# Optimization experiments

Measured on AMD Instinct MI355X. Metric: run time of the kernel, lower is better.

Reference implementation:

```python
import jax, jax.numpy as jnp
import numpy as np

DFAUD = 1024
DFRGB = 1024
DIM_K = 1024
N_HEADS = 4
B, T = 16, 1024


def setup_inputs() -> dict:
    key = jax.random.key(0)
    ks = jax.random.split(key, 11)
    s = lambda d: 1.0 / np.sqrt(d)
    return {
        "x": jax.random.normal(ks[0], (B, T, DFAUD), jnp.float32),
        "y": jax.random.normal(ks[1], (B, T, DFRGB), jnp.float32),
        "adj": jax.random.normal(ks[2], (B, T, T), jnp.float32),
        "Wq": jax.random.uniform(ks[3], (DIM_K, DFAUD), jnp.float32, -s(DFAUD), s(DFAUD)),
        "bq": jnp.zeros((DIM_K,), jnp.float32),
        "Wk": jax.random.uniform(ks[4], (DIM_K, DFRGB), jnp.float32, -s(DFRGB), s(DFRGB)),
        "bk": jnp.zeros((DIM_K,), jnp.float32),
        "Wv": jax.random.uniform(ks[5], (DIM_K, DFRGB), jnp.float32, -s(DFRGB), s(DFRGB)),
        "bv": jnp.zeros((DIM_K,), jnp.float32),
        "Wo": jax.random.uniform(ks[6], (DFRGB, DIM_K), jnp.float32, -s(DIM_K), s(DIM_K)),
        "bo": jnp.zeros((DFRGB,), jnp.float32),
    }


def reference(x, y, adj, Wq, bq, Wk, bk, Wv, bv, Wo, bo):
    b, t = x.shape[0], x.shape[1]
    dh = DIM_K // N_HEADS
    norm = 1.0 / np.sqrt(DIM_K)
    # Faithful reproduction of the torch reshape(-1, B, T, dim_k // n_heads):
    # [B, T, dim_k] -> [n_heads, B, T, dh] (row-major reshape, layout-mixing for h>1)
    Q = (x @ Wq.T + bq).reshape(N_HEADS, b, t, dh)
    K = (y @ Wk.T + bk).reshape(N_HEADS, b, t, dh)
    V = (y @ Wv.T + bv).reshape(N_HEADS, b, t, dh)
    scores = jnp.einsum('hbqd,hbkd->hbqk', Q, K) * norm  # [h, B, T, T]
    att = jax.nn.softmax(scores + adj, axis=-1)          # adj [B,T,T] broadcasts
    temp = jnp.einsum('hbqk,hbkd->hbqd', att, V).reshape(b, t, DIM_K)
    out = (temp @ Wo.T + bo).reshape(-1, t, y.shape[2])
    return out
```

## Files before the change

### kernel.cpp

```cpp
#include <hip/hip_runtime.h>
#include <stdint.h>

typedef unsigned short u16;
typedef __attribute__((ext_vector_type(8))) short short8_t;
typedef __attribute__((ext_vector_type(4))) float f32x4;

typedef const __attribute__((address_space(1))) void GV;
typedef __attribute__((address_space(3))) void LV;

__device__ __forceinline__ void gload_lds16(const void* g, void* l) {
  __builtin_amdgcn_global_load_lds((GV*)g, (LV*)l, 16, 0, 0);
}

__device__ __forceinline__ u16 f2bf(float f) {
  union { float f; uint32_t u; } v; v.f = f;
  return (u16)((v.u + 0x7FFFu + ((v.u >> 16) & 1u)) >> 16);
}

__device__ __forceinline__ f32x4 fz4() { f32x4 v = {0.f, 0.f, 0.f, 0.f}; return v; }

__global__ __launch_bounds__(256) void cast_kernel(const float* __restrict__ in,
                                                   u16* __restrict__ out) {
  int i = (blockIdx.x * 256 + threadIdx.x) * 4;
  float4 v = *(const float4*)(in + i);
  ushort4 o;
  o.x = f2bf(v.x); o.y = f2bf(v.y); o.z = f2bf(v.z); o.w = f2bf(v.w);
  *(ushort4*)(out + i) = o;
}

template <int OUT_BF16>
__global__ __launch_bounds__(512, 2) void gemm8(const u16* __restrict__ A,
                                                const u16* __restrict__ B,
                                                const float* __restrict__ bias,
                                                void* __restrict__ Cout,
                                                int M, int N, int K) {
  __shared__ u16 Al[2 * 16384];
  __shared__ u16 Bl[2 * 16384];
  const int tid = threadIdx.x, w = tid >> 6, l = tid & 63;
  const int g = l >> 4, q = l & 15;
  const int n0 = blockIdx.x * 256, m0 = blockIdx.y * 256;
  const int wr = (w >> 2) * 128, wc = (w & 3) * 64;
  const int NT = K >> 6;
  const int ah = w >> 2;
  const int bh = (w & 3) >> 1;
  const int brow0 = ((w & 3) & 1) * 64;

#define STAGE_A(S, half)                                                          \
  {                                                                               \
    _Pragma("unroll") for (int j_ = 0; j_ < 2; ++j_) {                            \
      const int idx_ = j_ * 512 + tid;                                            \
      const int row_ = idx_ >> 3;                                                 \
      const int sl_ = (idx_ & 7) ^ (((idx_ >> 5) & 1) << 1);                      \
      gload_lds16(A + (size_t)(m0 + (half) * 128 + row_) * K + (S) * 64 + sl_ * 8,\
                  Al + ((S) & 1) * 16384 + (half) * 8192 + (j_ * 512 + w * 64) * 8);\
    }                                                                             \
  }
#define STAGE_B(S, half)                                                          \
  {                                                                               \
    _Pragma("unroll") for (int j_ = 0; j_ < 2; ++j_) {                            \
      const int idx_ = j_ * 512 + tid;                                            \
      const int row_ = idx_ >> 3;                                                 \
      const int sl_ = (idx_ & 7) ^ (((idx_ >> 5) & 1) << 1);                      \
      gload_lds16(B + (size_t)(n0 + (half) * 128 + row_) * K + (S) * 64 + sl_ * 8,\
                  Bl + ((S) & 1) * 16384 + (half) * 8192 + (j_ * 512 + w * 64) * 8);\
    }                                                                             \
  }

  f32x4 acc[8][4];
#pragma unroll
  for (int i = 0; i < 8; ++i)
#pragma unroll
    for (int n = 0; n < 4; ++n) acc[i][n] = fz4();

  float bv[4];
#pragma unroll
  for (int nf = 0; nf < 4; ++nf) bv[nf] = bias[n0 + wc + nf * 16 + q];

  STAGE_A(0, 0); STAGE_A(0, 1); STAGE_B(0, 0); STAGE_B(0, 1);
  STAGE_A(1, 0); STAGE_A(1, 1); STAGE_B(1, 0); STAGE_B(1, 1);
  asm volatile("s_waitcnt vmcnt(8)");
  __builtin_amdgcn_s_barrier();

  short8_t bfr[4][2];
  for (int S = 0; S < NT; ++S) {
    const int bs = (S & 1) * 16384;
#pragma unroll
    for (int p = 0; p < 4; ++p) {
      short8_t afr[2][2];
#pragma unroll
      for (int mi = 0; mi < 2; ++mi)
#pragma unroll
        for (int kk = 0; kk < 2; ++kk) {
          const int r = (2 * p + mi) * 16 + q;
          afr[mi][kk] = *(const short8_t*)(Al + bs + ah * 8192 + r * 64 +
                                           ((kk * 4 + g) ^ (((r >> 2) & 1) << 1)) * 8);
        }
      if (p == 0) {
#pragma unroll
        for (int nf = 0; nf < 4; ++nf)
#pragma unroll
          for (int kk = 0; kk < 2; ++kk) {
            const int r = brow0 + nf * 16 + q;
            bfr[nf][kk] = *(const short8_t*)(Bl + bs + bh * 8192 + r * 64 +
                                             ((kk * 4 + g) ^ (((r >> 2) & 1) << 1)) * 8);
          }
      }
      if (p == 0 && S >= 1 && S + 1 < NT) STAGE_A(S + 1, 0);
      if (p == 1 && S >= 1 && S + 1 < NT) STAGE_A(S + 1, 1);
      if (p == 2 && S + 2 < NT) STAGE_B(S + 2, 0);
      if (p == 3 && S + 2 < NT) STAGE_B(S + 2, 1);
      if (p == 3) {
        if (S == NT - 2) { asm volatile("s_waitcnt vmcnt(0)"); }
        else if (S < NT - 2) { asm volatile("s_waitcnt vmcnt(4)"); }
      }
      __builtin_amdgcn_s_barrier();
      asm volatile("s_waitcnt lgkmcnt(0)" ::: "memory");
      __builtin_amdgcn_sched_barrier(0);
      __builtin_amdgcn_s_setprio(1);
#pragma unroll
      for (int nf = 0; nf < 4; ++nf)
#pragma unroll
        for (int mi = 0; mi < 2; ++mi)
#pragma unroll
          for (int kk = 0; kk < 2; ++kk)
            acc[2 * p + mi][nf] = __builtin_amdgcn_mfma_f32_16x16x32_bf16(
                afr[mi][kk], bfr[nf][kk], acc[2 * p + mi][nf], 0, 0, 0);
      __builtin_amdgcn_s_setprio(0);
      __builtin_amdgcn_s_barrier();
    }
  }
#undef STAGE_A
#undef STAGE_B

#pragma unroll
  for (int nf = 0; nf < 4; ++nf) {
    const int col = n0 + wc + nf * 16 + q;
#pragma unroll
    for (int mf = 0; mf < 8; ++mf) {
      const int rowb = m0 + wr + mf * 16 + g * 4;
#pragma unroll
      for (int j = 0; j < 4; ++j) {
        const float vv = acc[mf][nf][j] + bv[nf];
        if (OUT_BF16)
          ((u16*)Cout)[(size_t)(rowb + j) * N + col] = f2bf(vv);
        else
          ((float*)Cout)[(size_t)(rowb + j) * N + col] = vv;
      }
    }
  }
}

__global__ __launch_bounds__(256) void transpose_v(const u16* __restrict__ V,
                                                   u16* __restrict__ VT) {
  __shared__ u16 t[64][68];
  const int hb = blockIdx.z;
  const int t0 = blockIdx.x * 64, d0 = blockIdx.y * 64;
  const u16* src = V + (size_t)hb * 1024 * 256;
  u16* dst = VT + (size_t)hb * 256 * 1024;
  const int tid = threadIdx.x;
#pragma unroll
  for (int i = 0; i < 4; ++i) {
    const int idx = i * 256 + tid;
    const int r = idx >> 4, c4 = (idx & 15) * 4;
    ushort4 v = *(const ushort4*)(src + (size_t)(t0 + r) * 256 + d0 + c4);
    *(ushort4*)&t[r][c4] = v;
  }
  __syncthreads();
#pragma unroll
  for (int i = 0; i < 4; ++i) {
    const int idx = i * 256 + tid;
    const int r = idx >> 4, c4 = (idx & 15) * 4;
    ushort4 v;
    v.x = t[c4][r]; v.y = t[c4 + 1][r]; v.z = t[c4 + 2][r]; v.w = t[c4 + 3][r];
    *(ushort4*)(dst + (size_t)(d0 + r) * 1024 + t0 + c4) = v;
  }
}

__global__ __launch_bounds__(256) void attn_kernel(const u16* __restrict__ Q,
                                                   const u16* __restrict__ Kf,
                                                   const u16* __restrict__ VT,
                                                   const float* __restrict__ adj,
                                                   u16* __restrict__ O) {
  __shared__ u16 Ks[32 * 256];
  __shared__ u16 Vs[256 * 32];
  __shared__ u16 Ps[4][16 * 32];
  const int tid = threadIdx.x, w = tid >> 6, l = tid & 63;
  const int g = l >> 4, q = l & 15;
  const int bid = blockIdx.x;
  const int xcd = bid & 7, idx = bid >> 3;
  const int b = xcd * 2 + (idx >> 6);
  const int qb = (idx >> 2) & 15, h = idx & 3;
  const int hb = h * 16 + b;
  const int q0 = qb * 64;
  const u16* qb_p = Q + ((size_t)hb * 1024 + q0 + w * 16) * 256;
  const u16* kb = Kf + (size_t)hb * 1024 * 256;
  const u16* vtb = VT + (size_t)hb * 256 * 1024;
  const float* adjr = adj + (size_t)b * 1024 * 1024 + (size_t)(q0 + w * 16 + q) * 1024;

  const int krow_b = tid >> 5;
  const int kslot = tid & 31;
  const int vdr_b = tid >> 2;
  const int vsl = tid & 3;

  short8_t qf[8];
#pragma unroll
  for (int kk = 0; kk < 8; ++kk)
    qf[kk] = *(const short8_t*)(qb_p + (size_t)q * 256 + kk * 32 + g * 8);

  f32x4 o[16];
#pragma unroll
  for (int n = 0; n < 16; ++n) o[n] = fz4();
  float mrun = -1e30f, lrun = 0.f;

  short8_t kst[4], vst[4];

#define LOADREGS(ktt)                                                              \
  {                                                                                \
    _Pragma("unroll") for (int i_ = 0; i_ < 4; ++i_) {                             \
      const int row_ = i_ * 8 + krow_b;                                            \
      kst[i_] = *(const short8_t*)(kb + (size_t)((ktt) * 32 + row_) * 256 +        \
                                   kslot * 8);                                     \
    }                                                                              \
    _Pragma("unroll") for (int i_ = 0; i_ < 4; ++i_) {                             \
      const int dr_ = i_ * 64 + vdr_b;                                             \
      vst[i_] = *(const short8_t*)(vtb + (size_t)dr_ * 1024 + (ktt) * 32 +         \
                                   vsl * 8);                                       \
    }                                                                              \
  }
#define WRITEREGS()                                                                \
  {                                                                                \
    _Pragma("unroll") for (int i_ = 0; i_ < 4; ++i_) {                             \
      const int row_ = i_ * 8 + krow_b;                                            \
      *(short8_t*)((char*)Ks + row_ * 512 + ((kslot ^ (row_ & 7)) * 16)) = kst[i_];\
    }                                                                              \
    _Pragma("unroll") for (int i_ = 0; i_ < 4; ++i_) {                             \
      const int dr_ = i_ * 64 + vdr_b;                                             \
      *(short8_t*)((char*)Vs + dr_ * 64 + ((vsl ^ ((dr_ >> 1) & 3)) * 16)) = vst[i_];\
    }                                                                              \
  }

  LOADREGS(0);
  float4 a0 = *(const float4*)(adjr + 0 * 32 + 0 * 16 + g * 4);
  float4 a1 = *(const float4*)(adjr + 0 * 32 + 1 * 16 + g * 4);
  WRITEREGS();
  __syncthreads();

  for (int kt = 0; kt < 32; ++kt) {
    float4 n0v = a0, n1v = a1;
    if (kt < 31) {
      LOADREGS(kt + 1);
      n0v = *(const float4*)(adjr + (kt + 1) * 32 + 0 * 16 + g * 4);
      n1v = *(const float4*)(adjr + (kt + 1) * 32 + 1 * 16 + g * 4);
    }

    f32x4 s[2];
    __builtin_amdgcn_s_setprio(1);
#pragma unroll
    for (int f = 0; f < 2; ++f) {
      f32x4 a = fz4();
      const int row = f * 16 + q;
      const char* kr = (const char*)Ks + row * 512;
#pragma unroll
      for (int kk = 0; kk < 8; ++kk) {
        const int cb = kk * 64 + g * 16;
        short8_t kfr = *(const short8_t*)(kr + (cb ^ ((row & 7) << 4)));
        a = __builtin_amdgcn_mfma_f32_16x16x32_bf16(kfr, qf[kk], a, 0, 0, 0);
      }
      s[f] = a;
    }
    __builtin_amdgcn_s_setprio(0);

#pragma unroll
    for (int j = 0; j < 4; ++j) {
      s[0][j] = s[0][j] * 0.03125f + ((const float*)&a0)[j];
      s[1][j] = s[1][j] * 0.03125f + ((const float*)&a1)[j];
    }

    float pmax = s[0][0];
#pragma unroll
    for (int j = 1; j < 4; ++j) pmax = fmaxf(pmax, s[0][j]);
#pragma unroll
    for (int j = 0; j < 4; ++j) pmax = fmaxf(pmax, s[1][j]);
    pmax = fmaxf(pmax, __shfl_xor(pmax, 16));
    pmax = fmaxf(pmax, __shfl_xor(pmax, 32));

    if (!__all(pmax - mrun <= 8.0f)) {
      const float mn = fmaxf(mrun, pmax);
      const float al = __expf(mrun - mn);
      mrun = mn;
      lrun *= al;
#pragma unroll
      for (int n = 0; n < 16; ++n)
#pragma unroll
        for (int r = 0; r < 4; ++r) o[n][r] *= al;
    }

    float sum = 0.f;
#pragma unroll
    for (int f = 0; f < 2; ++f)
#pragma unroll
      for (int j = 0; j < 4; ++j) {
        const float p = __expf(s[f][j] - mrun);
        s[f][j] = p;
        sum += p;
      }
    sum += __shfl_xor(sum, 16);
    sum += __shfl_xor(sum, 32);
    lrun += sum;

    {
      char* pw = (char*)Ps[w] + q * 64;
      const int swz = (q >> 1) & 3;
#pragma unroll
      for (int f = 0; f < 2; ++f) {
        ushort4 pk;
        pk.x = f2bf(s[f][0]); pk.y = f2bf(s[f][1]);
        pk.z = f2bf(s[f][2]); pk.w = f2bf(s[f][3]);
        *(ushort4*)(pw + ((f * 32 + g * 8) ^ (swz << 4))) = pk;
      }
    }
    asm volatile("s_waitcnt lgkmcnt(0)");
    __builtin_amdgcn_sched_barrier(0);
    short8_t pa = *(const short8_t*)((const char*)Ps[w] + q * 64 +
                                     ((g * 16) ^ (((q >> 1) & 3) << 4)));

    __builtin_amdgcn_s_setprio(1);
#pragma unroll
    for (int n = 0; n < 16; ++n) {
      const int dr = n * 16 + q;
      const int sl = g ^ ((dr >> 1) & 3);
      short8_t vf = *(const short8_t*)((const char*)Vs + dr * 64 + sl * 16);
      o[n] = __builtin_amdgcn_mfma_f32_16x16x32_bf16(vf, pa, o[n], 0, 0, 0);
    }
    __builtin_amdgcn_s_setprio(0);

    if (kt < 31) {
      __syncthreads();
      WRITEREGS();
      __syncthreads();
    }
    a0 = n0v; a1 = n1v;
  }
#undef LOADREGS
#undef WRITEREGS

  const float inv = 1.0f / lrun;
  u16* ob = O + ((size_t)hb * 1024 + q0 + w * 16 + q) * 256;
#pragma unroll
  for (int n = 0; n < 16; ++n) {
    ushort4 st;
    st.x = f2bf(o[n][0] * inv); st.y = f2bf(o[n][1] * inv);
    st.z = f2bf(o[n][2] * inv); st.w = f2bf(o[n][3] * inv);
    *(ushort4*)(ob + n * 16 + g * 4) = st;
  }
}

extern "C" void kernel_launch(void* const* d_in, const int* in_sizes, int n_in,
                              void* d_out, int out_size, void* d_ws, size_t ws_size,
                              hipStream_t stream) {
  (void)in_sizes; (void)n_in; (void)out_size; (void)ws_size;
  const float* x   = (const float*)d_in[0];
  const float* y   = (const float*)d_in[1];
  const float* adj = (const float*)d_in[2];
  const float* Wq  = (const float*)d_in[3];
  const float* bq  = (const float*)d_in[4];
  const float* Wk  = (const float*)d_in[5];
  const float* bk  = (const float*)d_in[6];
  const float* Wv  = (const float*)d_in[7];
  const float* bv  = (const float*)d_in[8];
  const float* Wo  = (const float*)d_in[9];
  const float* bo  = (const float*)d_in[10];

  char* ws = (char*)d_ws;
  const size_t MB = 1ull << 20;
  u16* Xb  = (u16*)(ws + 0);
  u16* Yb  = (u16*)(ws + 32 * MB);
  u16* Wqb = (u16*)(ws + 64 * MB);
  u16* Wkb = (u16*)(ws + 66 * MB);
  u16* Wvb = (u16*)(ws + 68 * MB);
  u16* Wob = (u16*)(ws + 70 * MB);
  u16* Qb  = (u16*)(ws + 72 * MB);
  u16* Kb  = (u16*)(ws + 104 * MB);
  u16* Vb  = (u16*)(ws + 136 * MB);
  u16* VTb = (u16*)(ws + 168 * MB);
  u16* Tmp = Xb;

  cast_kernel<<<16384, 256, 0, stream>>>(x, Xb);
  cast_kernel<<<16384, 256, 0, stream>>>(y, Yb);
  cast_kernel<<<1024, 256, 0, stream>>>(Wq, Wqb);
  cast_kernel<<<1024, 256, 0, stream>>>(Wk, Wkb);
  cast_kernel<<<1024, 256, 0, stream>>>(Wv, Wvb);
  cast_kernel<<<1024, 256, 0, stream>>>(Wo, Wob);

  dim3 gg(4, 64);
  gemm8<1><<<gg, 512, 0, stream>>>(Xb, Wqb, bq, Qb, 16384, 1024, 1024);
  gemm8<1><<<gg, 512, 0, stream>>>(Yb, Wkb, bk, Kb, 16384, 1024, 1024);
  gemm8<1><<<gg, 512, 0, stream>>>(Yb, Wvb, bv, Vb, 16384, 1024, 1024);

  transpose_v<<<dim3(16, 4, 64), 256, 0, stream>>>(Vb, VTb);

  attn_kernel<<<1024, 256, 0, stream>>>(Qb, Kb, VTb, adj, Tmp);

  gemm8<0><<<gg, 512, 0, stream>>>(Tmp, Wob, bo, d_out, 16384, 1024, 1024);
}
```

Measured before the change: 376.0 us.

## Double the attention key tile to 64 and halve loop iterations

The flash-attention loop now processes 64 keys per iteration instead of 32. K, V and P tiles in LDS double in size, and the V/P swizzle layouts are redone for 128-byte rows. The PV product now issues two MFMAs per output fragment. This halves the number of barrier pairs and softmax-rescale passes per row block. The adj prefetch across iterations is replaced by loads at the top of each iteration, and the larger register staging and LDS footprint may reduce occupancy.

```diff
diff --git a/kernel.cpp b/kernel.cpp
--- a/kernel.cpp
+++ b/kernel.cpp
@@ -181,9 +181,9 @@
                                                    const u16* __restrict__ VT,
                                                    const float* __restrict__ adj,
                                                    u16* __restrict__ O) {
-  __shared__ u16 Ks[32 * 256];
-  __shared__ u16 Vs[256 * 32];
-  __shared__ u16 Ps[4][16 * 32];
+  __shared__ u16 Ks[64 * 256];
+  __shared__ u16 Vs[256 * 64];
+  __shared__ u16 Ps[4][16 * 64];
   const int tid = threadIdx.x, w = tid >> 6, l = tid & 63;
   const int g = l >> 4, q = l & 15;
   const int bid = blockIdx.x;
@@ -199,8 +199,8 @@
 
   const int krow_b = tid >> 5;
   const int kslot = tid & 31;
-  const int vdr_b = tid >> 2;
-  const int vsl = tid & 3;
+  const int vdr_b = tid >> 3;
+  const int vsl = tid & 7;
 
   short8_t qf[8];
 #pragma unroll
@@ -212,51 +212,48 @@
   for (int n = 0; n < 16; ++n) o[n] = fz4();
   float mrun = -1e30f, lrun = 0.f;
 
-  short8_t kst[4], vst[4];
+  short8_t kst[8], vst[8];
 
 #define LOADREGS(ktt)                                                              \
   {                                                                                \
-    _Pragma("unroll") for (int i_ = 0; i_ < 4; ++i_) {                             \
+    _Pragma("unroll") for (int i_ = 0; i_ < 8; ++i_) {                             \
       const int row_ = i_ * 8 + krow_b;                                            \
-      kst[i_] = *(const short8_t*)(kb + (size_t)((ktt) * 32 + row_) * 256 +        \
+      kst[i_] = *(const short8_t*)(kb + (size_t)((ktt) * 64 + row_) * 256 +        \
                                    kslot * 8);                                     \
     }                                                                              \
-    _Pragma("unroll") for (int i_ = 0; i_ < 4; ++i_) {                             \
-      const int dr_ = i_ * 64 + vdr_b;                                             \
-      vst[i_] = *(const short8_t*)(vtb + (size_t)dr_ * 1024 + (ktt) * 32 +         \
+    _Pragma("unroll") for (int i_ = 0; i_ < 8; ++i_) {                             \
+      const int dr_ = i_ * 32 + vdr_b;                                             \
+      vst[i_] = *(const short8_t*)(vtb + (size_t)dr_ * 1024 + (ktt) * 64 +         \
                                    vsl * 8);                                       \
     }                                                                              \
   }
 #define WRITEREGS()                                                                \
   {                                                                                \
-    _Pragma("unroll") for (int i_ = 0; i_ < 4; ++i_) {                             \
+    _Pragma("unroll") for (int i_ = 0; i_ < 8; ++i_) {                             \
       const int row_ = i_ * 8 + krow_b;                                            \
       *(short8_t*)((char*)Ks + row_ * 512 + ((kslot ^ (row_ & 7)) * 16)) = kst[i_];\
     }                                                                              \
-    _Pragma("unroll") for (int i_ = 0; i_ < 4; ++i_) {                             \
-      const int dr_ = i_ * 64 + vdr_b;                                             \
-      *(short8_t*)((char*)Vs + dr_ * 64 + ((vsl ^ ((dr_ >> 1) & 3)) * 16)) = vst[i_];\
+    _Pragma("unroll") for (int i_ = 0; i_ < 8; ++i_) {                             \
+      const int dr_ = i_ * 32 + vdr_b;                                             \
+      *(short8_t*)((char*)Vs + dr_ * 128 + ((vsl ^ (dr_ & 7)) * 16)) = vst[i_];    \
     }                                                                              \
   }
 
   LOADREGS(0);
-  float4 a0 = *(const float4*)(adjr + 0 * 32 + 0 * 16 + g * 4);
-  float4 a1 = *(const float4*)(adjr + 0 * 32 + 1 * 16 + g * 4);
   WRITEREGS();
   __syncthreads();
 
-  for (int kt = 0; kt < 32; ++kt) {
-    float4 n0v = a0, n1v = a1;
-    if (kt < 31) {
-      LOADREGS(kt + 1);
-      n0v = *(const float4*)(adjr + (kt + 1) * 32 + 0 * 16 + g * 4);
-      n1v = *(const float4*)(adjr + (kt + 1) * 32 + 1 * 16 + g * 4);
-    }
-
-    f32x4 s[2];
+  for (int kt = 0; kt < 16; ++kt) {
+    float4 af[4];
+#pragma unroll
+    for (int f = 0; f < 4; ++f)
+      af[f] = *(const float4*)(adjr + kt * 64 + f * 16 + g * 4);
+    if (kt < 15) LOADREGS(kt + 1);
+
+    f32x4 s[4];
     __builtin_amdgcn_s_setprio(1);
 #pragma unroll
-    for (int f = 0; f < 2; ++f) {
+    for (int f = 0; f < 4; ++f) {
       f32x4 a = fz4();
       const int row = f * 16 + q;
       const char* kr = (const char*)Ks + row * 512;
@@ -271,16 +268,16 @@
     __builtin_amdgcn_s_setprio(0);
 
 #pragma unroll
-    for (int j = 0; j < 4; ++j) {
-      s[0][j] = s[0][j] * 0.03125f + ((const float*)&a0)[j];
-      s[1][j] = s[1][j] * 0.03125f + ((const float*)&a1)[j];
-    }
+    for (int f = 0; f < 4; ++f)
+#pragma unroll
+      for (int j = 0; j < 4; ++j)
+        s[f][j] = s[f][j] * 0.03125f + ((const float*)&af[f])[j];
 
     float pmax = s[0][0];
 #pragma unroll
-    for (int j = 1; j < 4; ++j) pmax = fmaxf(pmax, s[0][j]);
-#pragma unroll
-    for (int j = 0; j < 4; ++j) pmax = fmaxf(pmax, s[1][j]);
+    for (int f = 0; f < 4; ++f)
+#pragma unroll
+      for (int j = 0; j < 4; ++j) pmax = fmaxf(pmax, s[f][j]);
     pmax = fmaxf(pmax, __shfl_xor(pmax, 16));
     pmax = fmaxf(pmax, __shfl_xor(pmax, 32));
 
@@ -297,7 +294,7 @@
 
     float sum = 0.f;
 #pragma unroll
-    for (int f = 0; f < 2; ++f)
+    for (int f = 0; f < 4; ++f)
 #pragma unroll
       for (int j = 0; j < 4; ++j) {
         const float p = __expf(s[f][j] - mrun);
@@ -309,37 +306,42 @@
     lrun += sum;
 
     {
-      char* pw = (char*)Ps[w] + q * 64;
-      const int swz = (q >> 1) & 3;
-#pragma unroll
-      for (int f = 0; f < 2; ++f) {
+      char* pw = (char*)Ps[w] + q * 128;
+      const int qs = q & 7;
+#pragma unroll
+      for (int f = 0; f < 4; ++f) {
         ushort4 pk;
         pk.x = f2bf(s[f][0]); pk.y = f2bf(s[f][1]);
         pk.z = f2bf(s[f][2]); pk.w = f2bf(s[f][3]);
-        *(ushort4*)(pw + ((f * 32 + g * 8) ^ (swz << 4))) = pk;
+        *(ushort4*)(pw + (((f * 2 + (g >> 1)) ^ qs) * 16) + ((g & 1) * 8)) = pk;
       }
     }
     asm volatile("s_waitcnt lgkmcnt(0)");
     __builtin_amdgcn_sched_barrier(0);
-    short8_t pa = *(const short8_t*)((const char*)Ps[w] + q * 64 +
-                                     ((g * 16) ^ (((q >> 1) & 3) << 4)));
+    short8_t pa[2];
+#pragma unroll
+    for (int kk = 0; kk < 2; ++kk)
+      pa[kk] = *(const short8_t*)((const char*)Ps[w] + q * 128 +
+                                  (((kk * 4 + g) ^ (q & 7)) * 16));
 
     __builtin_amdgcn_s_setprio(1);
 #pragma unroll
     for (int n = 0; n < 16; ++n) {
       const int dr = n * 16 + q;
-      const int sl = g ^ ((dr >> 1) & 3);
-      short8_t vf = *(const short8_t*)((const char*)Vs + dr * 64 + sl * 16);
-      o[n] = __builtin_amdgcn_mfma_f32_16x16x32_bf16(vf, pa, o[n], 0, 0, 0);
+      const char* vr = (const char*)Vs + dr * 128;
+#pragma unroll
+      for (int kk = 0; kk < 2; ++kk) {
+        short8_t vf = *(const short8_t*)(vr + (((kk * 4 + g) ^ (dr & 7)) * 16));
+        o[n] = __builtin_amdgcn_mfma_f32_16x16x32_bf16(vf, pa[kk], o[n], 0, 0, 0);
+      }
     }
     __builtin_amdgcn_s_setprio(0);
 
-    if (kt < 31) {
+    if (kt < 15) {
       __syncthreads();
       WRITEREGS();
       __syncthreads();
     }
-    a0 = n0v; a1 = n1v;
   }
 #undef LOADREGS
 #undef WRITEREGS
```

Measured after the change: 465.1 us. 23.7% more time.
